# Optimization experiments

Hardware: AMD Instinct MI355X
Metric: run time of the kernel (lower is better)

## Reference

```python
import jax, jax.numpy as jnp
import numpy as np
import math

B, N, T, CI, CO = 4, 2048, 64, 32, 32
K, TAU = 6, 3


def _cheb(x, gso, k_order):
    # x: [b,n,t,c] complex, gso: [n,n] complex -> [K,b,n,t,c]
    polys = [x]
    if k_order > 1:
        polys.append(jnp.einsum('nm,bmtc->bntc', gso, x))
    for _ in range(2, k_order):
        polys.append(2.0 * jnp.einsum('nm,bmtc->bntc', gso, polys[-1]) - polys[-2])
    return jnp.stack(polys)


def _lag(p, tau):
    # shift along time axis (-2) by tau, zero-padding at the front
    if tau == 0:
        return p
    pad = jnp.zeros_like(p[..., :tau, :])
    return jnp.concatenate([pad, p[..., :-tau, :]], axis=-2)


def setup_inputs() -> dict:
    key = jax.random.key(0)
    ks = jax.random.split(key, 6)
    scale = 1.0 / math.sqrt(K * TAU * CI)
    gso_scale = 0.5 / math.sqrt(N)  # keep spectral radius ~<=1 for Cheb recursion
    return {
        'x_real': jax.random.normal(ks[0], (B, N, T, CI), jnp.float32),
        'x_imag': jax.random.normal(ks[1], (B, N, T, CI), jnp.float32),
        'gso_real': jax.random.normal(ks[2], (N, N), jnp.float32) * gso_scale,
        'gso_imag': jax.random.normal(ks[3], (N, N), jnp.float32) * gso_scale,
        'weight_real': jax.random.uniform(ks[4], (K, TAU, CI, CO), jnp.float32, -scale, scale),
        'weight_imag': jax.random.uniform(ks[5], (K, TAU, CI, CO), jnp.float32, -scale, scale),
        'bias_real': jnp.zeros((CO,), jnp.float32),
        'bias_imag': jnp.zeros((CO,), jnp.float32),
    }


def reference(x_real, x_imag, gso_real, gso_imag, weight_real, weight_imag, bias_real, bias_imag):
    x = jax.lax.complex(x_real, x_imag)
    gso = jax.lax.complex(gso_real, gso_imag)
    w = jax.lax.complex(weight_real, weight_imag)  # [K,TAU,i,o]
    bias = jax.lax.complex(bias_real, bias_imag)
    # Lag (time shift) and the graph shift act on different axes, so they
    # commute: compute the Chebyshev recursion ONCE on x, then lag the
    # stacked polynomials — same math as cheb(lag(x)) in the original.
    polys = _cheb(x, gso, K)  # [K,b,n,t,c]
    out = jnp.zeros((B, N, T, CO), dtype=polys.dtype)
    for tau in range(TAU):
        out = out + jnp.einsum('kbnti,kio->bnto', _lag(polys, tau), w[:, tau])
    return out + bias
```

## Files before the change

### kernel.cpp

```cpp
#include <hip/hip_runtime.h>
#include <stdint.h>

#define Bn 4
#define Nn 2048
#define Tn 64
#define CIn 32
#define COn 32
#define Kn 6
#define TAUn 3
#define Jn 8192

typedef _Float16 f16;
typedef _Float16 f16x2 __attribute__((ext_vector_type(2)));
typedef _Float16 f16x4 __attribute__((ext_vector_type(4)));
typedef _Float16 f16x8 __attribute__((ext_vector_type(8)));
typedef float f32x4 __attribute__((ext_vector_type(4)));

#if defined(__has_builtin)
#if __has_builtin(__builtin_amdgcn_fdot2)
#define HAVE_FDOT2 1
#endif
#endif

__device__ __forceinline__ float fdot2(f16x2 a, f16x2 b, float c) {
#ifdef HAVE_FDOT2
  return __builtin_amdgcn_fdot2(a, b, c, false);
#else
  return c + (float)a[0] * (float)b[0] + (float)a[1] * (float)b[1];
#endif
}

__device__ __forceinline__ void gld_lds16(const void* g, void* l) {
  auto gp = (const __attribute__((address_space(1))) uint32_t*)(uintptr_t)g;
  auto lp = (__attribute__((address_space(3))) uint32_t*)(uint32_t)(uintptr_t)l;
  __builtin_amdgcn_global_load_lds(gp, lp, 16, 0, 0);
}

__global__ __launch_bounds__(256) void pack_gso(const float* __restrict__ gr,
                                                const float* __restrict__ gi,
                                                f16* __restrict__ Gr,
                                                f16* __restrict__ Gi) {
  int u = blockIdx.x * 256 + threadIdx.x;
  float4 vr = ((const float4*)gr)[u];
  float4 vi = ((const float4*)gi)[u];
  f16x4 hr, hi;
  hr[0] = (f16)vr.x; hr[1] = (f16)vr.y; hr[2] = (f16)vr.z; hr[3] = (f16)vr.w;
  hi[0] = (f16)vi.x; hi[1] = (f16)vi.y; hi[2] = (f16)vi.z; hi[3] = (f16)vi.w;
  ((f16x4*)Gr)[u] = hr;
  ((f16x4*)Gi)[u] = hi;
}

__global__ __launch_bounds__(256) void pack_x(const float* __restrict__ xr,
                                              const float* __restrict__ xi,
                                              f16* __restrict__ P0) {
  __shared__ float tile[64][65];
  const int t = threadIdx.x;
  const int q0 = blockIdx.x * 64;
  const int n0 = blockIdx.y * 64;
  const int b = blockIdx.z;
  const int rr = t >> 4;
  const int cc = (t & 15) * 4;
  #pragma unroll
  for (int plane = 0; plane < 2; ++plane) {
    const float* src = plane ? xi : xr;
    if (plane) __syncthreads();
    #pragma unroll
    for (int it = 0; it < 4; ++it) {
      int n = it * 16 + rr;
      float4 v = *(const float4*)(src + ((size_t)b * Nn + n0 + n) * 2048 + q0 + cc);
      tile[n][cc + 0] = v.x; tile[n][cc + 1] = v.y;
      tile[n][cc + 2] = v.z; tile[n][cc + 3] = v.w;
    }
    __syncthreads();
    #pragma unroll
    for (int it = 0; it < 4; ++it) {
      int q = it * 16 + rr;
      f16x4 hv;
      hv[0] = (f16)tile[cc + 0][q];
      hv[1] = (f16)tile[cc + 1][q];
      hv[2] = (f16)tile[cc + 2][q];
      hv[3] = (f16)tile[cc + 3][q];
      *(f16x4*)(P0 + ((size_t)b * 2048 + q0 + q) * 4096 + plane * 2048 + n0 + cc) = hv;
    }
  }
}

__global__ __launch_bounds__(256) void pack_w(const float* __restrict__ wr,
                                              const float* __restrict__ wi,
                                              uint2* __restrict__ wpk) {
  int idx = blockIdx.x * 256 + threadIdx.x;
  if (idx >= Kn * TAUn * CIn * COn) return;
  float r = wr[idx], i = wi[idx];
  uint16_t hr = __builtin_bit_cast(uint16_t, (f16)r);
  uint16_t hi = __builtin_bit_cast(uint16_t, (f16)i);
  uint16_t hni = __builtin_bit_cast(uint16_t, (f16)(-i));
  uint2 o;
  o.x = (uint32_t)hr | ((uint32_t)hni << 16);
  o.y = (uint32_t)hi | ((uint32_t)hr << 16);
  wpk[idx] = o;
}

template <int MODE>
__global__ __launch_bounds__(512, 2) void cheb_gemm(
    const f16* __restrict__ Gr, const f16* __restrict__ Gi,
    const f16* __restrict__ P, f16* __restrict__ Q) {
  extern __shared__ __align__(16) char lds[];
  f16* L = (f16*)lds;

  const int tid = threadIdx.x;
  const int lane = tid & 63;
  const int w = tid >> 6;
  const int wm = w >> 2;
  const int wn = w & 3;
  const int sub = lane >> 4, rr = lane & 15;

  const int bid = blockIdx.x;
  const int xcd = bid & 7;
  const int l = bid >> 3;
  const int bj = xcd * 4 + (l >> 4);
  const int bn = l & 15;
  const int n0 = bn * 256, j0 = bj * 256;
  const bool top = n0 < 2048;
  const int gmbase = n0 & 2047;

  auto stageA = [&](const f16* plane, int kcol, int h, int slot) {
    #pragma unroll
    for (int p = 0; p < 2; ++p) {
      int u = p * 512 + tid;
      int row = u & 127, c = u >> 7;
      const f16* src = plane + (size_t)(gmbase + h * 128 + row) * 2048 + kcol + c * 8;
      gld_lds16(src, L + slot * 8192 + (u - lane) * 8);
    }
  };
  auto stageB = [&](int kt, int h, int slot) {
    #pragma unroll
    for (int p = 0; p < 2; ++p) {
      int u = p * 512 + tid;
      int row = u & 127, c = u >> 7;
      const f16* src = P + (size_t)(j0 + h * 128 + row) * 4096 + kt * 64 + c * 8;
      gld_lds16(src, L + slot * 8192 + (u - lane) * 8);
    }
  };
  auto Aplane = [&](int kt) -> const f16* {
    bool kr = (kt & 32) != 0;
    return top ? (kr ? Gi : Gr) : (kr ? Gr : Gi);
  };

  f32x4 acc[8][4] = {};
  f16x8 afr[4][2], bfr0[2][2], bfr1[2][2];

  stageA(Aplane(0), 0, 0, 0);
  stageA(Aplane(0), 0, 1, 1);
  stageB(0, 0, 2);
  stageB(0, 1, 3);
  stageA(Aplane(1), 64, 0, 4);

  for (int kt = 0; kt < 64; ++kt) {
    const int base = (kt & 1) * 4;
    const int nbase = base ^ 4;
    const int ktn = (kt + 1) & 63;
    const int ktn2 = (kt + 2) & 63;
    const f16* apn = Aplane(ktn);
    const f16* apn2 = Aplane(ktn2);
    const int kcoln = (ktn * 64) & 2047;
    const int kcoln2 = (ktn2 * 64) & 2047;
    const bool negA = top && (kt & 32);
    const int Aslot = base + wm;
    const int Bslot = base + 2 + (wn >> 1);
    const int brow = (wn & 1) * 64;

    auto loadA = [&](int qm) {
      #pragma unroll
      for (int f = 0; f < 4; ++f)
        #pragma unroll
        for (int ks = 0; ks < 2; ++ks)
          afr[f][ks] = *(const f16x8*)(
              L + Aslot * 8192 + ((ks * 4 + sub) * 128 + qm * 64 + f * 16 + rr) * 8);
      if (negA) {
        #pragma unroll
        for (int f = 0; f < 4; ++f) { afr[f][0] = -afr[f][0]; afr[f][1] = -afr[f][1]; }
      }
    };
    auto loadB = [&](f16x8 (&bq)[2][2], int qn) {
      #pragma unroll
      for (int fc = 0; fc < 2; ++fc)
        #pragma unroll
        for (int ks = 0; ks < 2; ++ks)
          bq[fc][ks] = *(const f16x8*)(
              L + Bslot * 8192 + ((ks * 4 + sub) * 128 + brow + qn * 32 + fc * 16 + rr) * 8);
    };
    auto mf16 = [&](f16x8 (&bq)[2][2], int accR, int accC) {
      __builtin_amdgcn_s_setprio(1);
      #pragma unroll
      for (int f = 0; f < 4; ++f)
        #pragma unroll
        for (int fc = 0; fc < 2; ++fc)
          #pragma unroll
          for (int ks = 0; ks < 2; ++ks)
            acc[accR + f][accC + fc] = __builtin_amdgcn_mfma_f32_16x16x32_f16(
                afr[f][ks], bq[fc][ks], acc[accR + f][accC + fc], 0, 0, 0);
      __builtin_amdgcn_s_setprio(0);
    };

    asm volatile("s_waitcnt vmcnt(2)" ::: "memory");
    __builtin_amdgcn_s_barrier();

    loadA(0); loadB(bfr0, 0);
    stageA(apn, kcoln, 1, nbase + 1);
    __builtin_amdgcn_s_barrier();
    mf16(bfr0, 0, 0);
    __builtin_amdgcn_s_barrier();

    loadB(bfr1, 1);
    stageB(ktn, 0, nbase + 2);
    __builtin_amdgcn_s_barrier();
    mf16(bfr1, 0, 2);
    __builtin_amdgcn_s_barrier();

    loadA(1);
    stageB(ktn, 1, nbase + 3);
    __builtin_amdgcn_s_barrier();
    mf16(bfr1, 4, 2);
    __builtin_amdgcn_s_barrier();

    stageA(apn2, kcoln2, 0, base + 0);
    __builtin_amdgcn_s_barrier();
    mf16(bfr0, 4, 0);
    __builtin_amdgcn_s_barrier();
  }

  asm volatile("s_waitcnt vmcnt(0)" ::: "memory");

  #pragma unroll
  for (int fc = 0; fc < 4; ++fc) {
    size_t j = (size_t)j0 + wn * 64 + fc * 16 + (lane & 15);
    #pragma unroll
    for (int fr = 0; fr < 8; ++fr) {
      int nn = n0 + wm * 128 + fr * 16 + ((lane >> 4) << 2);
      size_t off = j * 4096 + nn;
      f16x4 v;
      if (MODE == 1) {
        f16x4 o = *(const f16x4*)(Q + off);
        #pragma unroll
        for (int r = 0; r < 4; ++r)
          v[r] = (f16)(2.0f * acc[fr][fc][r] - (float)o[r]);
      } else {
        #pragma unroll
        for (int r = 0; r < 4; ++r)
          v[r] = (f16)acc[fr][fc][r];
      }
      *(f16x4*)(Q + off) = v;
    }
  }
}

template <bool CPLX>
__global__ __launch_bounds__(256, 4) void contract_k(
    const f16* __restrict__ Pc, const uint2* __restrict__ wpk,
    const float* __restrict__ biasr, const float* __restrict__ biasi,
    float* __restrict__ out, int k) {
  __shared__ __align__(16) uint32_t Plds[96 * 64];
  __shared__ __align__(16) uint32_t WA[96 * 32];
  __shared__ __align__(16) uint32_t WB[CPLX ? 96 * 32 : 32];

  const int t = threadIdx.x;
  const int n0 = blockIdx.x * 64;
  const int tt = blockIdx.y;
  const int b = blockIdx.z;

  #pragma unroll
  for (int it = 0; it < 3; ++it) {
    int task = it * 256 + t;
    int row = task >> 3, oc = task & 7;
    int tp = (tt - 2) * 32 + row;
    uint4 ur = {0, 0, 0, 0}, ui = {0, 0, 0, 0};
    if (tp >= 0) {
      size_t goff = ((size_t)b * 2048 + tp) * 4096 + n0 + oc * 8;
      ur = *(const uint4*)(Pc + goff);
      ui = *(const uint4*)(Pc + goff + 2048);
    }
    uint32_t* dst = &Plds[row * 64 + oc * 8];
    dst[0] = (ur.x & 0xffffu) | (ui.x << 16);
    dst[1] = (ur.x >> 16) | (ui.x & 0xffff0000u);
    dst[2] = (ur.y & 0xffffu) | (ui.y << 16);
    dst[3] = (ur.y >> 16) | (ui.y & 0xffff0000u);
    dst[4] = (ur.z & 0xffffu) | (ui.z << 16);
    dst[5] = (ur.z >> 16) | (ui.z & 0xffff0000u);
    dst[6] = (ur.w & 0xffffu) | (ui.w << 16);
    dst[7] = (ur.w >> 16) | (ui.w & 0xffff0000u);
  }
  #pragma unroll
  for (int it = 0; it < 12; ++it) {
    int idx = it * 256 + t;
    int q = idx >> 5, o = idx & 31;
    int tau = 2 - (q >> 5), ci = q & 31;
    uint2 wv = wpk[((k * TAUn + tau) * CIn + ci) * COn + o];
    WA[idx] = wv.x;
    if (CPLX) WB[idx] = wv.y;
  }
  __syncthreads();

  const int no = t & 7, ng = t >> 3;
  float aR[8] = {0, 0, 0, 0, 0, 0, 0, 0};
  float aI[8] = {0, 0, 0, 0, 0, 0, 0, 0};
  for (int q = 0; q < 96; ++q) {
    uint2 pp = *(const uint2*)&Plds[q * 64 + ng * 2];
    f16x2 h0 = __builtin_bit_cast(f16x2, pp.x);
    f16x2 h1 = __builtin_bit_cast(f16x2, pp.y);
    uint4 wa = *(const uint4*)&WA[q * 32 + no * 4];
    const uint32_t* wap = &wa.x;
    #pragma unroll
    for (int c = 0; c < 4; ++c) {
      f16x2 wv = __builtin_bit_cast(f16x2, wap[c]);
      aR[c] = fdot2(h0, wv, aR[c]);
      aR[4 + c] = fdot2(h1, wv, aR[4 + c]);
    }
    if (CPLX) {
      uint4 wb = *(const uint4*)&WB[q * 32 + no * 4];
      const uint32_t* wbp = &wb.x;
      #pragma unroll
      for (int c = 0; c < 4; ++c) {
        f16x2 wv = __builtin_bit_cast(f16x2, wbp[c]);
        aI[c] = fdot2(h0, wv, aI[c]);
        aI[4 + c] = fdot2(h1, wv, aI[4 + c]);
      }
    }
  }

  #pragma unroll
  for (int a = 0; a < 2; ++a) {
    size_t n = (size_t)n0 + ng * 2 + a;
    size_t ob = (((size_t)b * Nn + n) * Tn + tt) * COn + no * 4;
    if (!CPLX) {
      float4 v;
      v.x = aR[a * 4 + 0]; v.y = aR[a * 4 + 1];
      v.z = aR[a * 4 + 2]; v.w = aR[a * 4 + 3];
      float4 cur;
      if (k == 0) cur = *(const float4*)(biasr + no * 4);
      else cur = *(const float4*)(out + ob);
      v.x += cur.x; v.y += cur.y; v.z += cur.z; v.w += cur.w;
      *(float4*)(out + ob) = v;
    } else {
      float* po = out + ob * 2;
      float4 lo, hi;
      lo.x = aR[a * 4 + 0]; lo.y = aI[a * 4 + 0];
      lo.z = aR[a * 4 + 1]; lo.w = aI[a * 4 + 1];
      hi.x = aR[a * 4 + 2]; hi.y = aI[a * 4 + 2];
      hi.z = aR[a * 4 + 3]; hi.w = aI[a * 4 + 3];
      float4 c0, c1;
      if (k == 0) {
        const float* pr = biasr + no * 4;
        const float* pi = biasi + no * 4;
        c0 = make_float4(pr[0], pi[0], pr[1], pi[1]);
        c1 = make_float4(pr[2], pi[2], pr[3], pi[3]);
      } else {
        c0 = *(const float4*)(po);
        c1 = *(const float4*)(po + 4);
      }
      lo.x += c0.x; lo.y += c0.y; lo.z += c0.z; lo.w += c0.w;
      hi.x += c1.x; hi.y += c1.y; hi.z += c1.z; hi.w += c1.w;
      *(float4*)(po) = lo;
      *(float4*)(po + 4) = hi;
    }
  }
}

extern "C" void kernel_launch(void* const* d_in, const int* in_sizes, int n_in,
                              void* d_out, int out_size, void* d_ws, size_t ws_size,
                              hipStream_t stream) {
  (void)in_sizes; (void)n_in;
  const float* xr = (const float*)d_in[0];
  const float* xi = (const float*)d_in[1];
  const float* gr = (const float*)d_in[2];
  const float* gi = (const float*)d_in[3];
  const float* wr = (const float*)d_in[4];
  const float* wi = (const float*)d_in[5];
  const float* biasr = (const float*)d_in[6];
  const float* biasi = (const float*)d_in[7];
  float* out = (float*)d_out;

  const size_t PPLANE = (size_t)Jn * 4096 * sizeof(f16);
  const size_t GPLANE = (size_t)Nn * Nn * sizeof(f16);
  const size_t WPK = (size_t)Kn * TAUn * CIn * COn * 8;
  if (ws_size < 2 * PPLANE + 2 * GPLANE + WPK) return;

  char* ws = (char*)d_ws;
  f16* P0 = (f16*)(ws);
  f16* P1 = (f16*)(ws + PPLANE);
  f16* Gr = (f16*)(ws + 2 * PPLANE);
  f16* Gi = (f16*)(ws + 2 * PPLANE + GPLANE);
  uint2* wpk = (uint2*)(ws + 2 * PPLANE + 2 * GPLANE);

  const bool cplx = (out_size == 2 * Bn * Nn * Tn * COn);

  pack_gso<<<dim3(4096), dim3(256), 0, stream>>>(gr, gi, Gr, Gi);
  pack_x<<<dim3(32, 32, 4), dim3(256), 0, stream>>>(xr, xi, P0);
  pack_w<<<dim3(72), dim3(256), 0, stream>>>(wr, wi, wpk);

  #define CONTRACT(KK, Pp)                                                         \
    do {                                                                           \
      if (cplx)                                                                    \
        contract_k<true><<<dim3(32, 64, 4), dim3(256), 0, stream>>>(               \
            Pp, wpk, biasr, biasi, out, KK);                                       \
      else                                                                         \
        contract_k<false><<<dim3(32, 64, 4), dim3(256), 0, stream>>>(              \
            Pp, wpk, biasr, biasi, out, KK);                                       \
    } while (0)

  CONTRACT(0, P0);
  cheb_gemm<0><<<dim3(512), dim3(512), 131072, stream>>>(Gr, Gi, P0, P1);
  CONTRACT(1, P1);
  cheb_gemm<1><<<dim3(512), dim3(512), 131072, stream>>>(Gr, Gi, P1, P0);
  CONTRACT(2, P0);
  cheb_gemm<1><<<dim3(512), dim3(512), 131072, stream>>>(Gr, Gi, P0, P1);
  CONTRACT(3, P1);
  cheb_gemm<1><<<dim3(512), dim3(512), 131072, stream>>>(Gr, Gi, P1, P0);
  CONTRACT(4, P0);
  cheb_gemm<1><<<dim3(512), dim3(512), 131072, stream>>>(Gr, Gi, P0, P1);
  CONTRACT(5, P1);
  #undef CONTRACT
}
```

Measured before the change: 2.041 ms.

## Unroll GEMM main loop by two with compile-time LDS slots and deeper B prefetch

```diff
diff --git a/kernel.cpp b/kernel.cpp
--- a/kernel.cpp
+++ b/kernel.cpp
@@ -15,6 +15,8 @@
 typedef _Float16 f16x4 __attribute__((ext_vector_type(4)));
 typedef _Float16 f16x8 __attribute__((ext_vector_type(8)));
 typedef float f32x4 __attribute__((ext_vector_type(4)));
+
+template <int N> struct ic { static constexpr int v = N; };
 
 #if defined(__has_builtin)
 #if __has_builtin(__builtin_amdgcn_fdot2)
@@ -123,110 +125,116 @@
   const bool top = n0 < 2048;
   const int gmbase = n0 & 2047;
 
+  const int aofs = sub * 1024 + rr * 8;
+  const int bofs = sub * 1024 + (wn & 1) * 512 + rr * 8;
+  const int srow = tid & 127, scol = (tid >> 7) * 8;
+  const size_t aoffg = (size_t)(gmbase + srow) * 2048 + scol;
+  const size_t boffg = (size_t)(j0 + srow) * 4096 + scol;
+  const int sdst = (tid - lane) * 8;
+
   auto stageA = [&](const f16* plane, int kcol, int h, int slot) {
     #pragma unroll
-    for (int p = 0; p < 2; ++p) {
-      int u = p * 512 + tid;
-      int row = u & 127, c = u >> 7;
-      const f16* src = plane + (size_t)(gmbase + h * 128 + row) * 2048 + kcol + c * 8;
-      gld_lds16(src, L + slot * 8192 + (u - lane) * 8);
-    }
+    for (int p = 0; p < 2; ++p)
+      gld_lds16(plane + aoffg + h * 262144 + kcol + p * 32,
+                L + slot * 8192 + sdst + p * 4096);
   };
-  auto stageB = [&](int kt, int h, int slot) {
-    #pragma unroll
-    for (int p = 0; p < 2; ++p) {
-      int u = p * 512 + tid;
-      int row = u & 127, c = u >> 7;
-      const f16* src = P + (size_t)(j0 + h * 128 + row) * 4096 + kt * 64 + c * 8;
-      gld_lds16(src, L + slot * 8192 + (u - lane) * 8);
-    }
+  auto stageB = [&](int kt_, int h, int slot) {
+    #pragma unroll
+    for (int p = 0; p < 2; ++p)
+      gld_lds16(P + boffg + h * 524288 + kt_ * 64 + p * 32,
+                L + slot * 8192 + sdst + p * 4096);
   };
-  auto Aplane = [&](int kt) -> const f16* {
-    bool kr = (kt & 32) != 0;
+  auto Aplane = [&](int kt_) -> const f16* {
+    bool kr = (kt_ & 32) != 0;
     return top ? (kr ? Gi : Gr) : (kr ? Gr : Gi);
   };
 
   f32x4 acc[8][4] = {};
   f16x8 afr[4][2], bfr0[2][2], bfr1[2][2];
 
+  stageB(0, 0, 2);
   stageA(Aplane(0), 0, 0, 0);
   stageA(Aplane(0), 0, 1, 1);
-  stageB(0, 0, 2);
   stageB(0, 1, 3);
+  stageB(1, 0, 6);
   stageA(Aplane(1), 64, 0, 4);
 
-  for (int kt = 0; kt < 64; ++kt) {
-    const int base = (kt & 1) * 4;
-    const int nbase = base ^ 4;
-    const int ktn = (kt + 1) & 63;
-    const int ktn2 = (kt + 2) & 63;
-    const f16* apn = Aplane(ktn);
-    const f16* apn2 = Aplane(ktn2);
-    const int kcoln = (ktn * 64) & 2047;
-    const int kcoln2 = (ktn2 * 64) & 2047;
-    const bool negA = top && (kt & 32);
-    const int Aslot = base + wm;
-    const int Bslot = base + 2 + (wn >> 1);
-    const int brow = (wn & 1) * 64;
-
-    auto loadA = [&](int qm) {
-      #pragma unroll
-      for (int f = 0; f < 4; ++f)
+  for (int k2 = 0; k2 < 32; ++k2) {
+    const int ktb = k2 * 2;
+
+    auto tile = [&](auto ec) {
+      constexpr int E = decltype(ec)::v;
+      const int kt = ktb + E;
+      const int ktn = (kt + 1) & 63;
+      const int ktn2 = (kt + 2) & 63;
+      const f16* apn = Aplane(ktn);
+      const f16* apn2 = Aplane(ktn2);
+      const int kcoln = (ktn * 64) & 2047;
+      const int kcoln2 = (ktn2 * 64) & 2047;
+      const bool negA = top && (kt & 32);
+
+      auto loadA = [&](int qm) {
         #pragma unroll
-        for (int ks = 0; ks < 2; ++ks)
-          afr[f][ks] = *(const f16x8*)(
-              L + Aslot * 8192 + ((ks * 4 + sub) * 128 + qm * 64 + f * 16 + rr) * 8);
-      if (negA) {
-        #pragma unroll
-        for (int f = 0; f < 4; ++f) { afr[f][0] = -afr[f][0]; afr[f][1] = -afr[f][1]; }
-      }
-    };
-    auto loadB = [&](f16x8 (&bq)[2][2], int qn) {
-      #pragma unroll
-      for (int fc = 0; fc < 2; ++fc)
-        #pragma unroll
-        for (int ks = 0; ks < 2; ++ks)
-          bq[fc][ks] = *(const f16x8*)(
-              L + Bslot * 8192 + ((ks * 4 + sub) * 128 + brow + qn * 32 + fc * 16 + rr) * 8);
-    };
-    auto mf16 = [&](f16x8 (&bq)[2][2], int accR, int accC) {
-      __builtin_amdgcn_s_setprio(1);
-      #pragma unroll
-      for (int f = 0; f < 4; ++f)
+        for (int f = 0; f < 4; ++f)
+          #pragma unroll
+          for (int ks = 0; ks < 2; ++ks)
+            afr[f][ks] = *(const f16x8*)(
+                L + (E * 4 + wm) * 8192 + aofs + ks * 4096 + qm * 512 + f * 128);
+        if (negA) {
+          #pragma unroll
+          for (int f = 0; f < 4; ++f) { afr[f][0] = -afr[f][0]; afr[f][1] = -afr[f][1]; }
+        }
+      };
+      auto loadB = [&](f16x8 (&bq)[2][2], int qn) {
         #pragma unroll
         for (int fc = 0; fc < 2; ++fc)
           #pragma unroll
           for (int ks = 0; ks < 2; ++ks)
-            acc[accR + f][accC + fc] = __builtin_amdgcn_mfma_f32_16x16x32_f16(
-                afr[f][ks], bq[fc][ks], acc[accR + f][accC + fc], 0, 0, 0);
-      __builtin_amdgcn_s_setprio(0);
+            bq[fc][ks] = *(const f16x8*)(
+                L + (E * 4 + 2 + (wn >> 1)) * 8192 + bofs + ks * 4096 + qn * 256 + fc * 128);
+      };
+      auto mf16 = [&](f16x8 (&bq)[2][2], int accR, int accC) {
+        __builtin_amdgcn_s_setprio(1);
+        #pragma unroll
+        for (int ks = 0; ks < 2; ++ks)
+          #pragma unroll
+          for (int f = 0; f < 4; ++f)
+            #pragma unroll
+            for (int fc = 0; fc < 2; ++fc)
+              acc[accR + f][accC + fc] = __builtin_amdgcn_mfma_f32_16x16x32_f16(
+                  afr[f][ks], bq[fc][ks], acc[accR + f][accC + fc], 0, 0, 0);
+        __builtin_amdgcn_s_setprio(0);
+      };
+
+      asm volatile("s_waitcnt vmcnt(4)" ::: "memory");
+      __builtin_amdgcn_s_barrier();
+
+      loadA(0); loadB(bfr0, 0);
+      stageA(apn, kcoln, 1, (E ^ 1) * 4 + 1);
+      __builtin_amdgcn_s_barrier();
+      mf16(bfr0, 0, 0);
+      __builtin_amdgcn_s_barrier();
+
+      loadB(bfr1, 1);
+      stageB(ktn, 1, (E ^ 1) * 4 + 3);
+      __builtin_amdgcn_s_barrier();
+      mf16(bfr1, 0, 2);
+      __builtin_amdgcn_s_barrier();
+
+      loadA(1);
+      stageB(ktn2, 0, E * 4 + 2);
+      __builtin_amdgcn_s_barrier();
+      mf16(bfr1, 4, 2);
+      __builtin_amdgcn_s_barrier();
+
+      stageA(apn2, kcoln2, 0, E * 4 + 0);
+      __builtin_amdgcn_s_barrier();
+      mf16(bfr0, 4, 0);
+      __builtin_amdgcn_s_barrier();
     };
 
-    asm volatile("s_waitcnt vmcnt(2)" ::: "memory");
-    __builtin_amdgcn_s_barrier();
-
-    loadA(0); loadB(bfr0, 0);
-    stageA(apn, kcoln, 1, nbase + 1);
-    __builtin_amdgcn_s_barrier();
-    mf16(bfr0, 0, 0);
-    __builtin_amdgcn_s_barrier();
-
-    loadB(bfr1, 1);
-    stageB(ktn, 0, nbase + 2);
-    __builtin_amdgcn_s_barrier();
-    mf16(bfr1, 0, 2);
-    __builtin_amdgcn_s_barrier();
-
-    loadA(1);
-    stageB(ktn, 1, nbase + 3);
-    __builtin_amdgcn_s_barrier();
-    mf16(bfr1, 4, 2);
-    __builtin_amdgcn_s_barrier();
-
-    stageA(apn2, kcoln2, 0, base + 0);
-    __builtin_amdgcn_s_barrier();
-    mf16(bfr0, 4, 0);
-    __builtin_amdgcn_s_barrier();
+    tile(ic<0>{});
+    tile(ic<1>{});
   }
 
   asm volatile("s_waitcnt vmcnt(0)" ::: "memory");
```

Measured after the change: 1.991 ms. -2.5%, faster.
